# Performance work log

Hardware: AMD Instinct MI355X
Metric: run time of the kernel (lower is better)

## Reference

```python
import jax, jax.numpy as jnp
import numpy as np

MAX_DEPTH = 11  # node positions < 2**11 = 2048


def setup_inputs() -> dict:
    key = jax.random.key(0)
    k1, k2, k3, k4, k5 = jax.random.split(key, 5)
    B, S, dim = 4, 1024, 64
    token_types = jax.random.randint(k1, (B, S), 0, 5).astype(jnp.int32)
    # token_values in [-1, 2]: -1 marks out-of-scope for scope tokens;
    # bop uses tv+1 (0..3), nop uses tv+5 (4..7) -- all in-range for the 11-row table
    token_values = (jax.random.randint(k2, (B, S), 0, 4) - 1).astype(jnp.int32)
    node_positions = jax.random.randint(k3, (B, S), 0, 2048).astype(jnp.int32)
    embed_table = jax.random.normal(k4, (11, dim), dtype=jnp.float32)
    # mirrors torch.rand(2,dim,dim).softmax(-1).cumsum(-1) init
    primitives_raw = jnp.cumsum(
        jax.nn.softmax(jax.random.uniform(k5, (2, dim, dim), dtype=jnp.float32), axis=-1),
        axis=-1)
    return {
        "token_types": token_types,
        "token_values": token_values,
        "node_positions": node_positions,
        "embed_table": embed_table,
        "primitives_raw": primitives_raw,
    }


def _forward(token_types, token_values, node_positions, embed_table, primitives_raw):
    dim = embed_table.shape[1]
    B, S = token_types.shape

    # primitives = expm(P - P^H) for each of the 2 generators
    herm = primitives_raw - jnp.swapaxes(primitives_raw, -1, -2)
    prims = jax.vmap(jax.scipy.linalg.expm)(herm)  # [2, dim, dim]

    # --- positional encodings via binary-path matrix products ---
    # path(pos) applies prims[pos%2], then prims[(pos//2)%2], ... until pos==1.
    # Equivalent to the original's per-unique-position masked-linear loop,
    # evaluated per token (== positional_encodings[inverse]).
    maps = jnp.broadcast_to(jnp.eye(dim, dtype=embed_table.dtype), (B, S, dim, dim))
    pos = node_positions
    for _ in range(MAX_DEPTH):
        active = pos > 1
        bit = (pos & 1).astype(jnp.int32)
        step_p = prims[bit]  # [B, S, dim, dim] gather of the per-step generator
        # linear(maps, prim) == maps @ prim.T, applied rowwise to each map matrix
        stepped = jnp.einsum('bsij,bskj->bsik', maps, step_p)
        maps = jnp.where(active[..., None, None], stepped, maps)
        pos = pos >> 1

    # --- content embeddings via masked gathers ---
    tt, tv = token_types, token_values
    sos = tt == 0
    bop = tt == 1
    nop = tt == 2
    scope = tt == 3
    oos = scope & (tv == -1)
    db = tt == 4
    idx = jnp.where(sos, 0,
          jnp.where(bop, tv + 1,
          jnp.where(nop, tv + 5,
          jnp.where(db, 8,
          jnp.where(oos, 10, 0)))))
    valid = sos | bop | nop | db | oos  # in-scope scope tokens stay zero
    content = jnp.where(valid[..., None], embed_table[idx], jnp.zeros((), embed_table.dtype))
    return content, maps


def reference(token_types, token_values, node_positions, embed_table, primitives_raw):
    return _forward(token_types, token_values, node_positions, embed_table, primitives_raw)
```

## Files before the change

### kernel.cpp

```cpp
#include <hip/hip_runtime.h>
#include <hip/hip_bf16.h>
#include <stdint.h>

typedef __attribute__((ext_vector_type(4))) float fx4;
typedef __attribute__((ext_vector_type(16))) float fx16;
typedef __attribute__((ext_vector_type(8))) short bx8;
typedef unsigned short u16;
typedef unsigned int u32;

#define LDW 72
#define PL (64 * LDW)
#define MAGIC 0x9E3779B9u


__device__ __forceinline__ u16 f2bf(float x) {
    u32 u = __float_as_uint(x);
    return (u16)((u + 0x7FFFu + ((u >> 16) & 1u)) >> 16);
}
__device__ __forceinline__ float bf2f(u16 h) { return __uint_as_float(((u32)h) << 16); }

__device__ __forceinline__ bx8 ld32(const u16* p, int band, int kc, int l) {
    return *(const bx8*)(p + (band * 32 + (l & 31)) * LDW + kc * 16 + (l >> 5) * 8);
}

__device__ __forceinline__ void mmS(const u16* z1h, const u16* z1l,
                                    const u16* z2h, const u16* z2l,
                                    int ti, int tj, int l, fx16& acc) {
#pragma unroll
    for (int i = 0; i < 16; ++i) acc[i] = 0.f;
#pragma unroll
    for (int kc = 0; kc < 4; ++kc) {
        bx8 ah = ld32(z1h, ti, kc, l), al = ld32(z1l, ti, kc, l);
        bx8 bh = ld32(z2h, tj, kc, l), bl = ld32(z2l, tj, kc, l);
        acc = __builtin_amdgcn_mfma_f32_32x32x16_bf16(ah, bh, acc, 0, 0, 0);
        acc = __builtin_amdgcn_mfma_f32_32x32x16_bf16(ah, bl, acc, 0, 0, 0);
        acc = __builtin_amdgcn_mfma_f32_32x32x16_bf16(al, bh, acc, 0, 0, 0);
    }
}

__device__ __forceinline__ void mmD(const u16* z1h, const u16* z1l,
                                    const u16* z2h, const u16* z2l,
                                    int ti, int tj, int l, fx16& a1, fx16& a2) {
#pragma unroll
    for (int i = 0; i < 16; ++i) { a1[i] = 0.f; a2[i] = 0.f; }
#pragma unroll
    for (int kc = 0; kc < 4; ++kc) {
        bx8 ah = ld32(z1h, ti, kc, l), al = ld32(z1l, ti, kc, l);
        bx8 bh = ld32(z2h, tj, kc, l), bl = ld32(z2l, tj, kc, l);
        a1 = __builtin_amdgcn_mfma_f32_32x32x16_bf16(ah, bh, a1, 0, 0, 0);
        a1 = __builtin_amdgcn_mfma_f32_32x32x16_bf16(ah, bl, a1, 0, 0, 0);
        a1 = __builtin_amdgcn_mfma_f32_32x32x16_bf16(al, bh, a1, 0, 0, 0);
        a2 = __builtin_amdgcn_mfma_f32_32x32x16_bf16(bh, ah, a2, 0, 0, 0);
        a2 = __builtin_amdgcn_mfma_f32_32x32x16_bf16(bh, al, a2, 0, 0, 0);
        a2 = __builtin_amdgcn_mfma_f32_32x32x16_bf16(bl, ah, a2, 0, 0, 0);
    }
}

__device__ __forceinline__ void stP(u16* hi, u16* lo, int TI, int TJ, int l, const fx16& a) {
    const int Ar = TJ * 32 + (l & 31);
    const int c0 = TI * 32 + 4 * (l >> 5);
#pragma unroll
    for (int q = 0; q < 4; ++q) {
        union { u16 u[4]; uint2 v; } H, L;
#pragma unroll
        for (int r = 0; r < 4; ++r) {
            float v = a[4 * q + r];
            u32 u = __float_as_uint(v);
            H.u[r] = (u16)(u >> 16);
            L.u[r] = f2bf(v - __uint_as_float(u & 0xFFFF0000u));
        }
        *(uint2*)(hi + Ar * LDW + c0 + q * 8) = H.v;
        *(uint2*)(lo + Ar * LDW + c0 + q * 8) = L.v;
    }
}

__device__ __forceinline__ void stG(u16* T, int TI, int TJ, int l, const fx16& a) {
    const int Ar = TJ * 32 + (l & 31);
    const int c0 = TI * 32 + 4 * (l >> 5);
#pragma unroll
    for (int q = 0; q < 4; ++q) {
        union { u16 u[4]; uint2 v; } pk;
#pragma unroll
        for (int r = 0; r < 4; ++r) pk.u[r] = f2bf(a[4 * q + r]);
        *(uint2*)(T + Ar * 64 + c0 + q * 8) = pk.v;
    }
}

__device__ __forceinline__ void epiT32(fx16& a, const float* __restrict__ P,
                                       int TI, int TJ, int l, float qa, float qb) {
    const int gc = TJ * 32 + (l & 31);
    const int r0 = TI * 32 + 4 * (l >> 5);
#pragma unroll
    for (int q = 0; q < 4; ++q)
#pragma unroll
        for (int r = 0; r < 4; ++r) {
            const int gr = r0 + q * 8 + r;
            float m = (P[gc * 64 + gr] - P[gr * 64 + gc]) * 0.03125f;
            a[4 * q + r] += qb * m + (gr == gc ? qa : 0.f);
        }
}
__device__ __forceinline__ void epiN32(fx16& a, const float* __restrict__ P,
                                       int TI, int TJ, int l, float qa, float qb) {
    const int gc = TJ * 32 + (l & 31);
    const int r0 = TI * 32 + 4 * (l >> 5);
#pragma unroll
    for (int q = 0; q < 4; ++q)
#pragma unroll
        for (int r = 0; r < 4; ++r) {
            const int gr = r0 + q * 8 + r;
            float m = (P[gr * 64 + gc] - P[gc * 64 + gr]) * 0.03125f;
            a[4 * q + r] += qb * m + (gr == gc ? qa : 0.f);
        }
}

__global__ __launch_bounds__(256) void tables_kernel(const float* __restrict__ praw,
                                                     u16* __restrict__ wsP,
                                                     u16* __restrict__ rm_bf,
                                                     u16* __restrict__ cm_bf,
                                                     u32* __restrict__ flags)
{
    __shared__ u16 S[8 * PL];
    const int p = blockIdx.x, tid = threadIdx.x;
    const int w = tid >> 6, l = tid & 63;
    const int ti = w & 1, tj = w >> 1;

    if (p < 2) {
        const int g = p;
        const float* P = praw + g * 4096;
        u16* p0h = S;            u16* p0l = S + PL;
        u16* p1h = S + 2 * PL;   u16* p1l = S + 3 * PL;
        u16* p2h = S + 4 * PL;   u16* p2l = S + 5 * PL;
        u16* p3h = S + 6 * PL;   u16* p3l = S + 7 * PL;

        for (int s = tid; s < 4096; s += 256) {
            const int r = s >> 6, c = s & 63;
            const float m = (P[r * 64 + c] - P[c * 64 + r]) * 0.03125f;
            u32 um = __float_as_uint(m);
            float lof = m - __uint_as_float(um & 0xFFFF0000u);
            u16 hh = (u16)(um >> 16), ll = f2bf(lof);
            p0h[r * LDW + c] = hh;  p0l[r * LDW + c] = ll;
            p1h[c * LDW + r] = hh;  p1l[c * LDW + r] = ll;
        }
        __syncthreads();

        fx16 acc, a1, a2;

        mmS(p1h, p1l, p0h, p0l, ti, tj, l, acc);
        stP(p2h, p2l, ti, tj, l, acc);
        {
            const float C8 = 2.48015873015873e-5f, C9 = 2.75573192239859e-6f;
            for (int s = tid; s < 4096; s += 256) {
                const int r = s >> 6, c = s & 63;
                float m = bf2f(p0h[r * LDW + c]) + bf2f(p0l[r * LDW + c]);
                float v = C9 * m + (r == c ? C8 : 0.f);
                u32 u = __float_as_uint(v);
                p3h[r * LDW + c] = (u16)(u >> 16);
                p3l[r * LDW + c] = f2bf(v - __uint_as_float(u & 0xFFFF0000u));
            }
        }
        __syncthreads();

        mmS(p2h, p2l, p3h, p3l, ti, tj, l, acc);
        epiT32(acc, P, ti, tj, l, 1.388888888888889e-3f, 1.984126984126984e-4f);
        stP(p0h, p0l, ti, tj, l, acc);
        __syncthreads();
        mmS(p2h, p2l, p0h, p0l, ti, tj, l, acc);
        epiT32(acc, P, ti, tj, l, 4.166666666666667e-2f, 8.333333333333333e-3f);
        stP(p3h, p3l, ti, tj, l, acc);
        __syncthreads();
        mmS(p2h, p2l, p3h, p3l, ti, tj, l, acc);
        epiT32(acc, P, ti, tj, l, 0.5f, 1.666666666666667e-1f);
        stP(p0h, p0l, ti, tj, l, acc);
        __syncthreads();
        mmD(p2h, p2l, p0h, p0l, ti, tj, l, a1, a2);
        epiT32(a1, P, ti, tj, l, 1.f, 1.f);
        epiN32(a2, P, tj, ti, l, 1.f, 1.f);
        stP(p3h, p3l, ti, tj, l, a1);
        stP(p1h, p1l, tj, ti, l, a2);
        __syncthreads();

        u16 *Ych = p1h, *Ycl = p1l, *Xch = p3h, *Xcl = p3l;
        u16 *Ynh = p2h, *Ynl = p2l, *Xnh = p0h, *Xnl = p0l;
#pragma unroll 1
        for (int s5 = 0; s5 < 5; ++s5) {
            mmD(Ych, Ycl, Xch, Xcl, ti, tj, l, a1, a2);
            stP(Xnh, Xnl, ti, tj, l, a1);
            stP(Ynh, Ynl, tj, ti, l, a2);
            __syncthreads();
            u16* t;
            t = Xch; Xch = Xnh; Xnh = t;   t = Xcl; Xcl = Xnl; Xnl = t;
            t = Ych; Ych = Ynh; Ynh = t;   t = Ycl; Ycl = Ynl; Ynl = t;
        }

        for (int s8 = tid; s8 < 512; s8 += 256) {
            const int base = s8 * 8, r = base >> 6, c = base & 63;
            u16* dst = wsP + g * 16384;
            *(uint4*)(dst + base)         = *(const uint4*)(Ych + r * LDW + c);
            *(uint4*)(dst + 4096 + base)  = *(const uint4*)(Ycl + r * LDW + c);
            *(uint4*)(dst + 8192 + base)  = *(const uint4*)(Xch + r * LDW + c);
            *(uint4*)(dst + 12288 + base) = *(const uint4*)(Xcl + r * LDW + c);
        }
        __threadfence();
        __syncthreads();
        if (tid == 0) atomicExch(&flags[g], MAGIC);

        for (int s = tid; s < 4096; s += 256) {
            u16 v = ((s >> 6) == (s & 63)) ? (u16)0x3F80 : (u16)0;
            rm_bf[p * 4096 + s] = v;
            cm_bf[p * 4096 + s] = v;
        }
        return;
    }

    if (l == 0) {
        while (atomicOr(&flags[0], 0u) != MAGIC) __builtin_amdgcn_s_sleep(4);
        while (atomicOr(&flags[1], 0u) != MAGIC) __builtin_amdgcn_s_sleep(4);
    }
    __syncthreads();
    __threadfence();

    const int d = 31 - __clz(p);

    if (d == 1) {
        const u16* src = wsP + (p & 1) * 16384;
        for (int s = tid; s < 4096; s += 256) {
            rm_bf[p * 4096 + s] = f2bf(bf2f(src[s]) + bf2f(src[4096 + s]));
            cm_bf[p * 4096 + s] = f2bf(bf2f(src[8192 + s]) + bf2f(src[12288 + s]));
        }
        return;
    }

    u16* TAh = S;            u16* TAl = S + PL;
    u16* TBh = S + 2 * PL;   u16* TBl = S + 3 * PL;
    u16* Eah = S + 4 * PL;   u16* Eal = S + 5 * PL;
    u16* Ebh = S + 6 * PL;   u16* Ebl = S + 7 * PL;

    {
        const int b0 = p & 1;
        for (int s8 = tid; s8 < 512; s8 += 256) {
            const int base = s8 * 8, r = base >> 6, c = base & 63;
            *(uint4*)(TAh + r * LDW + c) = *(const uint4*)(wsP + 8192 + base);
            *(uint4*)(TAl + r * LDW + c) = *(const uint4*)(wsP + 12288 + base);
            *(uint4*)(TBh + r * LDW + c) = *(const uint4*)(wsP + 16384 + 8192 + base);
            *(uint4*)(TBl + r * LDW + c) = *(const uint4*)(wsP + 16384 + 12288 + base);
            *(uint4*)(Eah + r * LDW + c) = *(const uint4*)(wsP + b0 * 16384 + base);
            *(uint4*)(Eal + r * LDW + c) = *(const uint4*)(wsP + b0 * 16384 + 4096 + base);
        }
    }
    __syncthreads();

    fx16 acc, a1, a2;
    u16 *Ech = Eah, *Ecl = Eal, *Enh = Ebh, *Enl = Ebl;
#pragma unroll 1
    for (int j = 1; j <= d - 2; ++j) {
        const int b = (p >> j) & 1;
        mmS(b ? TBh : TAh, b ? TBl : TAl, Ech, Ecl, ti, tj, l, acc);
        stP(Enh, Enl, ti, tj, l, acc);
        __syncthreads();
        u16* t;
        t = Ech; Ech = Enh; Enh = t;   t = Ecl; Ecl = Enl; Enl = t;
    }
    {
        const int b = (p >> (d - 1)) & 1;
        mmD(b ? TBh : TAh, b ? TBl : TAl, Ech, Ecl, ti, tj, l, a1, a2);
        stG(rm_bf + p * 4096, ti, tj, l, a1);
        stG(cm_bf + p * 4096, tj, ti, l, a2);
    }
}

__global__ __launch_bounds__(256) void out_kernel(const int* __restrict__ tt,
                                                  const int* __restrict__ tv,
                                                  const int* __restrict__ npos,
                                                  const float* __restrict__ embed,
                                                  const u16* __restrict__ rm_bf,
                                                  const u16* __restrict__ cm_bf,
                                                  float* __restrict__ out)
{
    __shared__ float ST[4][16 * 64];
    const int tid = threadIdx.x;
    const int wv = tid >> 6, l = tid & 63;
    const int flat = blockIdx.x * 4 + wv;
    const int pos = npos[flat];

    {
        const int t = tt[flat], v = tv[flat];
        int idx; bool valid = true;
        if (t == 0)      idx = 0;
        else if (t == 1) idx = v + 1;
        else if (t == 2) idx = v + 5;
        else if (t == 4) idx = 8;
        else if (t == 3 && v == -1) idx = 10;
        else { idx = 0; valid = false; }
        out[flat * 64 + l] = valid ? embed[idx * 64 + l] : 0.f;
    }

    float* om = out + 4096 * 64 + (size_t)flat * 4096;

    if (pos < 64) {
        const u16* src = rm_bf + pos * 4096;
#pragma unroll
        for (int i = 0; i < 16; ++i) {
            const int f0 = i * 256 + l * 4;
            uint2 ld = *(const uint2*)(src + f0);
            fx4 v;
            v[0] = __uint_as_float(ld.x << 16); v[1] = __uint_as_float(ld.x & 0xFFFF0000u);
            v[2] = __uint_as_float(ld.y << 16); v[3] = __uint_as_float(ld.y & 0xFFFF0000u);
            *(fx4*)(om + f0) = v;
        }
    } else {
        const int lo5 = (pos & 31) | 32;
        const int hi5 = pos >> 5;
        const u16* Acm = cm_bf + hi5 * 4096;
        const u16* Brm = rm_bf + lo5 * 4096;
        const int lr = l & 15, h = l >> 4, k8 = h * 8;
        float* st = ST[wv];

        bx8 A0[4], A1[4], B0[4], B1[4];
#pragma unroll
        for (int q = 0; q < 4; ++q) {
            A0[q] = *(const bx8*)(Acm + (q * 16 + lr) * 64 + k8);
            A1[q] = *(const bx8*)(Acm + (q * 16 + lr) * 64 + 32 + k8);
        }
#pragma unroll
        for (int c = 0; c < 4; ++c) {
            B0[c] = *(const bx8*)(Brm + (c * 16 + lr) * 64 + k8);
            B1[c] = *(const bx8*)(Brm + (c * 16 + lr) * 64 + 32 + k8);
        }
#pragma unroll
        for (int ct = 0; ct < 4; ++ct) {
#pragma unroll
            for (int q = 0; q < 4; ++q) {
                fx4 c4 = { 0.f, 0.f, 0.f, 0.f };
                c4 = __builtin_amdgcn_mfma_f32_16x16x32_bf16(A0[q], B0[ct], c4, 0, 0, 0);
                c4 = __builtin_amdgcn_mfma_f32_16x16x32_bf16(A1[q], B1[ct], c4, 0, 0, 0);
                *(fx4*)(st + lr * 64 + 4 * ((4 * q + h) ^ lr)) = c4;
            }
#pragma unroll
            for (int i2 = 0; i2 < 4; ++i2) {
                const int row = i2 * 4 + h;
                fx4 v = *(const fx4*)(st + row * 64 + 4 * ((l & 15) ^ row));
                *(fx4*)(om + ct * 1024 + i2 * 256 + l * 4) = v;
            }
        }
    }
}

extern "C" void kernel_launch(void* const* d_in, const int* in_sizes, int n_in,
                              void* d_out, int out_size, void* d_ws, size_t ws_size,
                              hipStream_t stream)
{
    const int*   tt    = (const int*)d_in[0];
    const int*   tv    = (const int*)d_in[1];
    const int*   np    = (const int*)d_in[2];
    const float* embed = (const float*)d_in[3];
    const float* praw  = (const float*)d_in[4];
    float* out = (float*)d_out;

    u32* flags = (u32*)d_ws;
    u16* wsP   = (u16*)((char*)d_ws + 128);
    u16* rm_bf = (u16*)((char*)d_ws + 128 + 65536);
    u16* cm_bf = (u16*)((char*)d_ws + 128 + 65536 + 524288);

    tables_kernel<<<dim3(64), dim3(256), 0, stream>>>(praw, wsP, rm_bf, cm_bf, flags);
    out_kernel<<<dim3(1024), dim3(256), 0, stream>>>(tt, tv, np, embed, rm_bf, cm_bf, out);
}
```

Baseline: 42.25 us.

## Fuse table build and output expansion into one persistent kernel with per-table flags

Merges the table-building kernel and the output kernel into a single 512-block launch. Table blocks publish a per-position ready flag, and output blocks spin on only the tables they need, so token expansion can overlap with table construction. This removes the second launch and the serialization between the two kernels. In exchange it adds flag polling, relies on all blocks being co-resident to avoid deadlock, and gives each output block 9 tokens instead of 4.

```diff
diff --git a/kernel.cpp b/kernel.cpp
--- a/kernel.cpp
+++ b/kernel.cpp
@@ -113,19 +113,101 @@
         }
 }
 
-__global__ __launch_bounds__(256) void tables_kernel(const float* __restrict__ praw,
-                                                     u16* __restrict__ wsP,
-                                                     u16* __restrict__ rm_bf,
-                                                     u16* __restrict__ cm_bf,
-                                                     u32* __restrict__ flags)
+__device__ __forceinline__ void spinf(u32* f) {
+    while (atomicOr(f, 0u) != MAGIC) __builtin_amdgcn_s_sleep(2);
+}
+
+__device__ __forceinline__ void do_token(int flat, bool ready,
+        const int* __restrict__ tt, const int* __restrict__ tv,
+        const int* __restrict__ npos, const float* __restrict__ embed,
+        const u16* __restrict__ rm_bf, const u16* __restrict__ cm_bf,
+        float* __restrict__ out, u32* __restrict__ tflag, float* st, int l)
+{
+    const int pos = npos[flat];
+    if (!ready) {
+        if (l == 0) {
+            if (pos < 64) spinf(&tflag[pos]);
+            else { spinf(&tflag[(pos & 31) | 32]); spinf(&tflag[pos >> 5]); }
+        }
+        __threadfence();
+    }
+
+    {
+        const int t = tt[flat], v = tv[flat];
+        int idx; bool valid = true;
+        if (t == 0)      idx = 0;
+        else if (t == 1) idx = v + 1;
+        else if (t == 2) idx = v + 5;
+        else if (t == 4) idx = 8;
+        else if (t == 3 && v == -1) idx = 10;
+        else { idx = 0; valid = false; }
+        out[flat * 64 + l] = valid ? embed[idx * 64 + l] : 0.f;
+    }
+
+    float* om = out + 4096 * 64 + (size_t)flat * 4096;
+
+    if (pos < 64) {
+        const u16* src = rm_bf + pos * 4096;
+#pragma unroll
+        for (int i = 0; i < 16; ++i) {
+            const int f0 = i * 256 + l * 4;
+            uint2 ld = *(const uint2*)(src + f0);
+            fx4 v;
+            v[0] = __uint_as_float(ld.x << 16); v[1] = __uint_as_float(ld.x & 0xFFFF0000u);
+            v[2] = __uint_as_float(ld.y << 16); v[3] = __uint_as_float(ld.y & 0xFFFF0000u);
+            *(fx4*)(om + f0) = v;
+        }
+    } else {
+        const int lo5 = (pos & 31) | 32;
+        const int hi5 = pos >> 5;
+        const u16* Acm = cm_bf + hi5 * 4096;
+        const u16* Brm = rm_bf + lo5 * 4096;
+        const int lr = l & 15, h = l >> 4, k8 = h * 8;
+
+        bx8 A0[4], A1[4], B0[4], B1[4];
+#pragma unroll
+        for (int q = 0; q < 4; ++q) {
+            A0[q] = *(const bx8*)(Acm + (q * 16 + lr) * 64 + k8);
+            A1[q] = *(const bx8*)(Acm + (q * 16 + lr) * 64 + 32 + k8);
+        }
+#pragma unroll
+        for (int c = 0; c < 4; ++c) {
+            B0[c] = *(const bx8*)(Brm + (c * 16 + lr) * 64 + k8);
+            B1[c] = *(const bx8*)(Brm + (c * 16 + lr) * 64 + 32 + k8);
+        }
+#pragma unroll
+        for (int ct = 0; ct < 4; ++ct) {
+#pragma unroll
+            for (int q = 0; q < 4; ++q) {
+                fx4 c4 = { 0.f, 0.f, 0.f, 0.f };
+                c4 = __builtin_amdgcn_mfma_f32_16x16x32_bf16(A0[q], B0[ct], c4, 0, 0, 0);
+                c4 = __builtin_amdgcn_mfma_f32_16x16x32_bf16(A1[q], B1[ct], c4, 0, 0, 0);
+                *(fx4*)(st + lr * 64 + 4 * ((4 * q + h) ^ lr)) = c4;
+            }
+#pragma unroll
+            for (int i2 = 0; i2 < 4; ++i2) {
+                const int row = i2 * 4 + h;
+                fx4 v = *(const fx4*)(st + row * 64 + 4 * ((l & 15) ^ row));
+                *(fx4*)(om + ct * 1024 + i2 * 256 + l * 4) = v;
+            }
+        }
+    }
+}
+
+__global__ __launch_bounds__(256) void fused_kernel(
+        const int* __restrict__ tt, const int* __restrict__ tv,
+        const int* __restrict__ npos, const float* __restrict__ embed,
+        const float* __restrict__ praw, float* __restrict__ out,
+        u16* __restrict__ wsP, u16* __restrict__ rm_bf, u16* __restrict__ cm_bf,
+        u32* __restrict__ gflag, u32* __restrict__ tflag)
 {
     __shared__ u16 S[8 * PL];
-    const int p = blockIdx.x, tid = threadIdx.x;
+    const int b = blockIdx.x, tid = threadIdx.x;
     const int w = tid >> 6, l = tid & 63;
     const int ti = w & 1, tj = w >> 1;
 
-    if (p < 2) {
-        const int g = p;
+    if (b < 2) {
+        const int g = b;
         const float* P = praw + g * 4096;
         u16* p0h = S;            u16* p0l = S + PL;
         u16* p1h = S + 2 * PL;   u16* p1l = S + 3 * PL;
@@ -202,146 +284,89 @@
         }
         __threadfence();
         __syncthreads();
-        if (tid == 0) atomicExch(&flags[g], MAGIC);
+        if (tid == 0) atomicExch(&gflag[g], MAGIC);
 
         for (int s = tid; s < 4096; s += 256) {
             u16 v = ((s >> 6) == (s & 63)) ? (u16)0x3F80 : (u16)0;
-            rm_bf[p * 4096 + s] = v;
-            cm_bf[p * 4096 + s] = v;
-        }
-        return;
-    }
-
-    if (l == 0) {
-        while (atomicOr(&flags[0], 0u) != MAGIC) __builtin_amdgcn_s_sleep(4);
-        while (atomicOr(&flags[1], 0u) != MAGIC) __builtin_amdgcn_s_sleep(4);
-    }
-    __syncthreads();
+            rm_bf[b * 4096 + s] = v;
+            cm_bf[b * 4096 + s] = v;
+        }
+        __threadfence();
+        __syncthreads();
+        if (tid == 0) atomicExch(&tflag[b], MAGIC);
+    } else if (b < 64) {
+        const int p = b;
+        if (l == 0) { spinf(&gflag[0]); spinf(&gflag[1]); }
+        __syncthreads();
+        __threadfence();
+
+        const int d = 31 - __clz(p);
+
+        if (d == 1) {
+            const u16* src = wsP + (p & 1) * 16384;
+            for (int s = tid; s < 4096; s += 256) {
+                rm_bf[p * 4096 + s] = f2bf(bf2f(src[s]) + bf2f(src[4096 + s]));
+                cm_bf[p * 4096 + s] = f2bf(bf2f(src[8192 + s]) + bf2f(src[12288 + s]));
+            }
+        } else {
+            u16* TAh = S;            u16* TAl = S + PL;
+            u16* TBh = S + 2 * PL;   u16* TBl = S + 3 * PL;
+            u16* Eah = S + 4 * PL;   u16* Eal = S + 5 * PL;
+            u16* Ebh = S + 6 * PL;   u16* Ebl = S + 7 * PL;
+
+            {
+                const int b0 = p & 1;
+                for (int s8 = tid; s8 < 512; s8 += 256) {
+                    const int base = s8 * 8, r = base >> 6, c = base & 63;
+                    *(uint4*)(TAh + r * LDW + c) = *(const uint4*)(wsP + 8192 + base);
+                    *(uint4*)(TAl + r * LDW + c) = *(const uint4*)(wsP + 12288 + base);
+                    *(uint4*)(TBh + r * LDW + c) = *(const uint4*)(wsP + 16384 + 8192 + base);
+                    *(uint4*)(TBl + r * LDW + c) = *(const uint4*)(wsP + 16384 + 12288 + base);
+                    *(uint4*)(Eah + r * LDW + c) = *(const uint4*)(wsP + b0 * 16384 + base);
+                    *(uint4*)(Eal + r * LDW + c) = *(const uint4*)(wsP + b0 * 16384 + 4096 + base);
+                }
+            }
+            __syncthreads();
+
+            fx16 acc, a1, a2;
+            u16 *Ech = Eah, *Ecl = Eal, *Enh = Ebh, *Enl = Ebl;
+#pragma unroll 1
+            for (int j = 1; j <= d - 2; ++j) {
+                const int bb = (p >> j) & 1;
+                mmS(bb ? TBh : TAh, bb ? TBl : TAl, Ech, Ecl, ti, tj, l, acc);
+                stP(Enh, Enl, ti, tj, l, acc);
+                __syncthreads();
+                u16* t;
+                t = Ech; Ech = Enh; Enh = t;   t = Ecl; Ecl = Enl; Enl = t;
+            }
+            {
+                const int bb = (p >> (d - 1)) & 1;
+                mmD(bb ? TBh : TAh, bb ? TBl : TAl, Ech, Ecl, ti, tj, l, a1, a2);
+                stG(rm_bf + p * 4096, ti, tj, l, a1);
+                stG(cm_bf + p * 4096, tj, ti, l, a2);
+            }
+        }
+        __threadfence();
+        __syncthreads();
+        if (tid == 0) atomicExch(&tflag[p], MAGIC);
+    }
+
+    if (b < 64) __syncthreads();
+
+    float* st = ((float*)S) + w * 1024;
+
+    u32 fv = (l < 64) ? atomicOr(&tflag[l], 0u) : MAGIC;
+    const bool ready = __all(fv == MAGIC);
     __threadfence();
 
-    const int d = 31 - __clz(p);
-
-    if (d == 1) {
-        const u16* src = wsP + (p & 1) * 16384;
-        for (int s = tid; s < 4096; s += 256) {
-            rm_bf[p * 4096 + s] = f2bf(bf2f(src[s]) + bf2f(src[4096 + s]));
-            cm_bf[p * 4096 + s] = f2bf(bf2f(src[8192 + s]) + bf2f(src[12288 + s]));
-        }
-        return;
-    }
-
-    u16* TAh = S;            u16* TAl = S + PL;
-    u16* TBh = S + 2 * PL;   u16* TBl = S + 3 * PL;
-    u16* Eah = S + 4 * PL;   u16* Eal = S + 5 * PL;
-    u16* Ebh = S + 6 * PL;   u16* Ebl = S + 7 * PL;
-
-    {
-        const int b0 = p & 1;
-        for (int s8 = tid; s8 < 512; s8 += 256) {
-            const int base = s8 * 8, r = base >> 6, c = base & 63;
-            *(uint4*)(TAh + r * LDW + c) = *(const uint4*)(wsP + 8192 + base);
-            *(uint4*)(TAl + r * LDW + c) = *(const uint4*)(wsP + 12288 + base);
-            *(uint4*)(TBh + r * LDW + c) = *(const uint4*)(wsP + 16384 + 8192 + base);
-            *(uint4*)(TBl + r * LDW + c) = *(const uint4*)(wsP + 16384 + 12288 + base);
-            *(uint4*)(Eah + r * LDW + c) = *(const uint4*)(wsP + b0 * 16384 + base);
-            *(uint4*)(Eal + r * LDW + c) = *(const uint4*)(wsP + b0 * 16384 + 4096 + base);
-        }
-    }
-    __syncthreads();
-
-    fx16 acc, a1, a2;
-    u16 *Ech = Eah, *Ecl = Eal, *Enh = Ebh, *Enl = Ebl;
+    if (b < 64) {
+        if (w == 0)
+            do_token(4032 + b, ready, tt, tv, npos, embed, rm_bf, cm_bf, out, tflag, st, l);
+    } else {
+        const int base = (b - 64) * 9;
 #pragma unroll 1
-    for (int j = 1; j <= d - 2; ++j) {
-        const int b = (p >> j) & 1;
-        mmS(b ? TBh : TAh, b ? TBl : TAl, Ech, Ecl, ti, tj, l, acc);
-        stP(Enh, Enl, ti, tj, l, acc);
-        __syncthreads();
-        u16* t;
-        t = Ech; Ech = Enh; Enh = t;   t = Ecl; Ecl = Enl; Enl = t;
-    }
-    {
-        const int b = (p >> (d - 1)) & 1;
-        mmD(b ? TBh : TAh, b ? TBl : TAl, Ech, Ecl, ti, tj, l, a1, a2);
-        stG(rm_bf + p * 4096, ti, tj, l, a1);
-        stG(cm_bf + p * 4096, tj, ti, l, a2);
-    }
-}
-
-__global__ __launch_bounds__(256) void out_kernel(const int* __restrict__ tt,
-                                                  const int* __restrict__ tv,
-                                                  const int* __restrict__ npos,
-                                                  const float* __restrict__ embed,
-                                                  const u16* __restrict__ rm_bf,
-                                                  const u16* __restrict__ cm_bf,
-                                                  float* __restrict__ out)
-{
-    __shared__ float ST[4][16 * 64];
-    const int tid = threadIdx.x;
-    const int wv = tid >> 6, l = tid & 63;
-    const int flat = blockIdx.x * 4 + wv;
-    const int pos = npos[flat];
-
-    {
-        const int t = tt[flat], v = tv[flat];
-        int idx; bool valid = true;
-        if (t == 0)      idx = 0;
-        else if (t == 1) idx = v + 1;
-        else if (t == 2) idx = v + 5;
-        else if (t == 4) idx = 8;
-        else if (t == 3 && v == -1) idx = 10;
-        else { idx = 0; valid = false; }
-        out[flat * 64 + l] = valid ? embed[idx * 64 + l] : 0.f;
-    }
-
-    float* om = out + 4096 * 64 + (size_t)flat * 4096;
-
-    if (pos < 64) {
-        const u16* src = rm_bf + pos * 4096;
-#pragma unroll
-        for (int i = 0; i < 16; ++i) {
-            const int f0 = i * 256 + l * 4;
-            uint2 ld = *(const uint2*)(src + f0);
-            fx4 v;
-            v[0] = __uint_as_float(ld.x << 16); v[1] = __uint_as_float(ld.x & 0xFFFF0000u);
-            v[2] = __uint_as_float(ld.y << 16); v[3] = __uint_as_float(ld.y & 0xFFFF0000u);
-            *(fx4*)(om + f0) = v;
-        }
-    } else {
-        const int lo5 = (pos & 31) | 32;
-        const int hi5 = pos >> 5;
-        const u16* Acm = cm_bf + hi5 * 4096;
-        const u16* Brm = rm_bf + lo5 * 4096;
-        const int lr = l & 15, h = l >> 4, k8 = h * 8;
-        float* st = ST[wv];
-
-        bx8 A0[4], A1[4], B0[4], B1[4];
-#pragma unroll
-        for (int q = 0; q < 4; ++q) {
-            A0[q] = *(const bx8*)(Acm + (q * 16 + lr) * 64 + k8);
-            A1[q] = *(const bx8*)(Acm + (q * 16 + lr) * 64 + 32 + k8);
-        }
-#pragma unroll
-        for (int c = 0; c < 4; ++c) {
-            B0[c] = *(const bx8*)(Brm + (c * 16 + lr) * 64 + k8);
-            B1[c] = *(const bx8*)(Brm + (c * 16 + lr) * 64 + 32 + k8);
-        }
-#pragma unroll
-        for (int ct = 0; ct < 4; ++ct) {
-#pragma unroll
-            for (int q = 0; q < 4; ++q) {
-                fx4 c4 = { 0.f, 0.f, 0.f, 0.f };
-                c4 = __builtin_amdgcn_mfma_f32_16x16x32_bf16(A0[q], B0[ct], c4, 0, 0, 0);
-                c4 = __builtin_amdgcn_mfma_f32_16x16x32_bf16(A1[q], B1[ct], c4, 0, 0, 0);
-                *(fx4*)(st + lr * 64 + 4 * ((4 * q + h) ^ lr)) = c4;
-            }
-#pragma unroll
-            for (int i2 = 0; i2 < 4; ++i2) {
-                const int row = i2 * 4 + h;
-                fx4 v = *(const fx4*)(st + row * 64 + 4 * ((l & 15) ^ row));
-                *(fx4*)(om + ct * 1024 + i2 * 256 + l * 4) = v;
-            }
-        }
+        for (int t = w; t < 9; t += 4)
+            do_token(base + t, ready, tt, tv, npos, embed, rm_bf, cm_bf, out, tflag, st, l);
     }
 }
 
@@ -356,11 +381,12 @@
     const float* praw  = (const float*)d_in[4];
     float* out = (float*)d_out;
 
-    u32* flags = (u32*)d_ws;
-    u16* wsP   = (u16*)((char*)d_ws + 128);
-    u16* rm_bf = (u16*)((char*)d_ws + 128 + 65536);
-    u16* cm_bf = (u16*)((char*)d_ws + 128 + 65536 + 524288);
-
-    tables_kernel<<<dim3(64), dim3(256), 0, stream>>>(praw, wsP, rm_bf, cm_bf, flags);
-    out_kernel<<<dim3(1024), dim3(256), 0, stream>>>(tt, tv, np, embed, rm_bf, cm_bf, out);
-}
+    u32* gflag = (u32*)d_ws;
+    u32* tflag = (u32*)((char*)d_ws + 256);
+    u16* wsP   = (u16*)((char*)d_ws + 1024);
+    u16* rm_bf = (u16*)((char*)d_ws + 1024 + 65536);
+    u16* cm_bf = (u16*)((char*)d_ws + 1024 + 65536 + 524288);
+
+    fused_kernel<<<dim3(512), dim3(256), 0, stream>>>(tt, tv, np, embed, praw, out,
+                                                      wsP, rm_bf, cm_bf, gflag, tflag);
+}
```

Measured after the change: 74.31 us. +75.9%, slower.

## Split MFMA accumulators, cache generator in LDS, spread spin flags per block

Applied to the files above, without the earlier changes.

Each split-bf16 product term now goes into its own MFMA accumulator, and the three are summed at the end. This breaks the serial dependency chain between back-to-back MFMAs. The scaled skew-symmetric generator is stored once in an fp32 LDS array, so the epilogues and the C9 step stop re-reading global memory and re-decoding the bf16 pair. The single pair of completion flags becomes 64 cache-line-separated flags per generator, so the waiting blocks poll distinct lines instead of contending on one address. The trade-off is more registers and extra LDS per block, which could lower occupancy.

```diff
diff --git a/kernel.cpp b/kernel.cpp
--- a/kernel.cpp
+++ b/kernel.cpp
@@ -26,33 +26,45 @@
 __device__ __forceinline__ void mmS(const u16* z1h, const u16* z1l,
                                     const u16* z2h, const u16* z2l,
                                     int ti, int tj, int l, fx16& acc) {
-#pragma unroll
-    for (int i = 0; i < 16; ++i) acc[i] = 0.f;
+    fx16 chh, chl, clh;
+#pragma unroll
+    for (int i = 0; i < 16; ++i) { chh[i] = 0.f; chl[i] = 0.f; clh[i] = 0.f; }
 #pragma unroll
     for (int kc = 0; kc < 4; ++kc) {
         bx8 ah = ld32(z1h, ti, kc, l), al = ld32(z1l, ti, kc, l);
         bx8 bh = ld32(z2h, tj, kc, l), bl = ld32(z2l, tj, kc, l);
-        acc = __builtin_amdgcn_mfma_f32_32x32x16_bf16(ah, bh, acc, 0, 0, 0);
-        acc = __builtin_amdgcn_mfma_f32_32x32x16_bf16(ah, bl, acc, 0, 0, 0);
-        acc = __builtin_amdgcn_mfma_f32_32x32x16_bf16(al, bh, acc, 0, 0, 0);
-    }
+        chh = __builtin_amdgcn_mfma_f32_32x32x16_bf16(ah, bh, chh, 0, 0, 0);
+        chl = __builtin_amdgcn_mfma_f32_32x32x16_bf16(ah, bl, chl, 0, 0, 0);
+        clh = __builtin_amdgcn_mfma_f32_32x32x16_bf16(al, bh, clh, 0, 0, 0);
+    }
+#pragma unroll
+    for (int i = 0; i < 16; ++i) acc[i] = chh[i] + (chl[i] + clh[i]);
 }
 
 __device__ __forceinline__ void mmD(const u16* z1h, const u16* z1l,
                                     const u16* z2h, const u16* z2l,
                                     int ti, int tj, int l, fx16& a1, fx16& a2) {
-#pragma unroll
-    for (int i = 0; i < 16; ++i) { a1[i] = 0.f; a2[i] = 0.f; }
+    fx16 c1a, c1b, c1c, c2a, c2b, c2c;
+#pragma unroll
+    for (int i = 0; i < 16; ++i) {
+        c1a[i] = 0.f; c1b[i] = 0.f; c1c[i] = 0.f;
+        c2a[i] = 0.f; c2b[i] = 0.f; c2c[i] = 0.f;
+    }
 #pragma unroll
     for (int kc = 0; kc < 4; ++kc) {
         bx8 ah = ld32(z1h, ti, kc, l), al = ld32(z1l, ti, kc, l);
         bx8 bh = ld32(z2h, tj, kc, l), bl = ld32(z2l, tj, kc, l);
-        a1 = __builtin_amdgcn_mfma_f32_32x32x16_bf16(ah, bh, a1, 0, 0, 0);
-        a1 = __builtin_amdgcn_mfma_f32_32x32x16_bf16(ah, bl, a1, 0, 0, 0);
-        a1 = __builtin_amdgcn_mfma_f32_32x32x16_bf16(al, bh, a1, 0, 0, 0);
-        a2 = __builtin_amdgcn_mfma_f32_32x32x16_bf16(bh, ah, a2, 0, 0, 0);
-        a2 = __builtin_amdgcn_mfma_f32_32x32x16_bf16(bh, al, a2, 0, 0, 0);
-        a2 = __builtin_amdgcn_mfma_f32_32x32x16_bf16(bl, ah, a2, 0, 0, 0);
+        c1a = __builtin_amdgcn_mfma_f32_32x32x16_bf16(ah, bh, c1a, 0, 0, 0);
+        c1b = __builtin_amdgcn_mfma_f32_32x32x16_bf16(ah, bl, c1b, 0, 0, 0);
+        c1c = __builtin_amdgcn_mfma_f32_32x32x16_bf16(al, bh, c1c, 0, 0, 0);
+        c2a = __builtin_amdgcn_mfma_f32_32x32x16_bf16(bh, ah, c2a, 0, 0, 0);
+        c2b = __builtin_amdgcn_mfma_f32_32x32x16_bf16(bh, al, c2b, 0, 0, 0);
+        c2c = __builtin_amdgcn_mfma_f32_32x32x16_bf16(bl, ah, c2c, 0, 0, 0);
+    }
+#pragma unroll
+    for (int i = 0; i < 16; ++i) {
+        a1[i] = c1a[i] + (c1b[i] + c1c[i]);
+        a2[i] = c2a[i] + (c2b[i] + c2c[i]);
     }
 }
 
@@ -86,7 +98,7 @@
     }
 }
 
-__device__ __forceinline__ void epiT32(fx16& a, const float* __restrict__ P,
+__device__ __forceinline__ void epiT32(fx16& a, const float* Mf,
                                        int TI, int TJ, int l, float qa, float qb) {
     const int gc = TJ * 32 + (l & 31);
     const int r0 = TI * 32 + 4 * (l >> 5);
@@ -95,11 +107,11 @@
 #pragma unroll
         for (int r = 0; r < 4; ++r) {
             const int gr = r0 + q * 8 + r;
-            float m = (P[gc * 64 + gr] - P[gr * 64 + gc]) * 0.03125f;
+            float m = Mf[gc * 65 + gr];
             a[4 * q + r] += qb * m + (gr == gc ? qa : 0.f);
         }
 }
-__device__ __forceinline__ void epiN32(fx16& a, const float* __restrict__ P,
+__device__ __forceinline__ void epiN32(fx16& a, const float* Mf,
                                        int TI, int TJ, int l, float qa, float qb) {
     const int gc = TJ * 32 + (l & 31);
     const int r0 = TI * 32 + 4 * (l >> 5);
@@ -108,7 +120,7 @@
 #pragma unroll
         for (int r = 0; r < 4; ++r) {
             const int gr = r0 + q * 8 + r;
-            float m = (P[gr * 64 + gc] - P[gc * 64 + gr]) * 0.03125f;
+            float m = Mf[gr * 65 + gc];
             a[4 * q + r] += qb * m + (gr == gc ? qa : 0.f);
         }
 }
@@ -120,6 +132,7 @@
                                                      u32* __restrict__ flags)
 {
     __shared__ u16 S[8 * PL];
+    __shared__ float Mf[64 * 65];
     const int p = blockIdx.x, tid = threadIdx.x;
     const int w = tid >> 6, l = tid & 63;
     const int ti = w & 1, tj = w >> 1;
@@ -135,6 +148,7 @@
         for (int s = tid; s < 4096; s += 256) {
             const int r = s >> 6, c = s & 63;
             const float m = (P[r * 64 + c] - P[c * 64 + r]) * 0.03125f;
+            Mf[r * 65 + c] = m;
             u32 um = __float_as_uint(m);
             float lof = m - __uint_as_float(um & 0xFFFF0000u);
             u16 hh = (u16)(um >> 16), ll = f2bf(lof);
@@ -151,8 +165,7 @@
             const float C8 = 2.48015873015873e-5f, C9 = 2.75573192239859e-6f;
             for (int s = tid; s < 4096; s += 256) {
                 const int r = s >> 6, c = s & 63;
-                float m = bf2f(p0h[r * LDW + c]) + bf2f(p0l[r * LDW + c]);
-                float v = C9 * m + (r == c ? C8 : 0.f);
+                float v = C9 * Mf[r * 65 + c] + (r == c ? C8 : 0.f);
                 u32 u = __float_as_uint(v);
                 p3h[r * LDW + c] = (u16)(u >> 16);
                 p3l[r * LDW + c] = f2bf(v - __uint_as_float(u & 0xFFFF0000u));
@@ -161,20 +174,20 @@
         __syncthreads();
 
         mmS(p2h, p2l, p3h, p3l, ti, tj, l, acc);
-        epiT32(acc, P, ti, tj, l, 1.388888888888889e-3f, 1.984126984126984e-4f);
+        epiT32(acc, Mf, ti, tj, l, 1.388888888888889e-3f, 1.984126984126984e-4f);
         stP(p0h, p0l, ti, tj, l, acc);
         __syncthreads();
         mmS(p2h, p2l, p0h, p0l, ti, tj, l, acc);
-        epiT32(acc, P, ti, tj, l, 4.166666666666667e-2f, 8.333333333333333e-3f);
+        epiT32(acc, Mf, ti, tj, l, 4.166666666666667e-2f, 8.333333333333333e-3f);
         stP(p3h, p3l, ti, tj, l, acc);
         __syncthreads();
         mmS(p2h, p2l, p3h, p3l, ti, tj, l, acc);
-        epiT32(acc, P, ti, tj, l, 0.5f, 1.666666666666667e-1f);
+        epiT32(acc, Mf, ti, tj, l, 0.5f, 1.666666666666667e-1f);
         stP(p0h, p0l, ti, tj, l, acc);
         __syncthreads();
         mmD(p2h, p2l, p0h, p0l, ti, tj, l, a1, a2);
-        epiT32(a1, P, ti, tj, l, 1.f, 1.f);
-        epiN32(a2, P, tj, ti, l, 1.f, 1.f);
+        epiT32(a1, Mf, ti, tj, l, 1.f, 1.f);
+        epiN32(a2, Mf, tj, ti, l, 1.f, 1.f);
         stP(p3h, p3l, ti, tj, l, a1);
         stP(p1h, p1l, tj, ti, l, a2);
         __syncthreads();
@@ -202,7 +215,7 @@
         }
         __threadfence();
         __syncthreads();
-        if (tid == 0) atomicExch(&flags[g], MAGIC);
+        if (tid < 64) atomicExch(&flags[(g * 64 + tid) * 32], MAGIC);
 
         for (int s = tid; s < 4096; s += 256) {
             u16 v = ((s >> 6) == (s & 63)) ? (u16)0x3F80 : (u16)0;
@@ -212,9 +225,9 @@
         return;
     }
 
-    if (l == 0) {
-        while (atomicOr(&flags[0], 0u) != MAGIC) __builtin_amdgcn_s_sleep(4);
-        while (atomicOr(&flags[1], 0u) != MAGIC) __builtin_amdgcn_s_sleep(4);
+    if (tid == 0) {
+        while (atomicOr(&flags[(0 * 64 + p) * 32], 0u) != MAGIC) __builtin_amdgcn_s_sleep(8);
+        while (atomicOr(&flags[(1 * 64 + p) * 32], 0u) != MAGIC) __builtin_amdgcn_s_sleep(8);
     }
     __syncthreads();
     __threadfence();
@@ -357,9 +370,9 @@
     float* out = (float*)d_out;
 
     u32* flags = (u32*)d_ws;
-    u16* wsP   = (u16*)((char*)d_ws + 128);
-    u16* rm_bf = (u16*)((char*)d_ws + 128 + 65536);
-    u16* cm_bf = (u16*)((char*)d_ws + 128 + 65536 + 524288);
+    u16* wsP   = (u16*)((char*)d_ws + 16384);
+    u16* rm_bf = (u16*)((char*)d_ws + 16384 + 65536);
+    u16* cm_bf = (u16*)((char*)d_ws + 16384 + 65536 + 524288);
 
     tables_kernel<<<dim3(64), dim3(256), 0, stream>>>(praw, wsP, rm_bf, cm_bf, flags);
     out_kernel<<<dim3(1024), dim3(256), 0, stream>>>(tt, tv, np, embed, rm_bf, cm_bf, out);
```

Result: faster. 40.05 us (-5.2%).
